# Optimization experiments

Hardware: AMD Instinct MI355X
Metric: run time of the kernel (lower is better)

Reference implementation:

```python
import jax, jax.numpy as jnp
from jax import lax
import numpy as np

B, C, T = 256, 64, 4096   # batch, in_channels, seq_len
H, K, NBLK, O = 64, 2, 4, 64  # hidden_channels, kernel, blocks, out_channels


def _conv1d(x, w, b, stride=1):
    # x: [N,C,T], w: [Cout,Cin,K], b: [Cout]
    y = lax.conv_general_dilated(x, w, window_strides=(stride,), padding='VALID',
                                 dimension_numbers=('NCH', 'OIH', 'NCH'))
    return y + b[None, :, None]


def setup_inputs() -> dict:
    key = jax.random.key(0)
    ks = jax.random.split(key, 12)
    s = 0.05  # small init so relu/sigmoid stay in sane range across 4 blocks
    return {
        'x': jax.random.normal(ks[0], (B, C, T), jnp.float32),
        'sig_w': jax.random.normal(ks[1], (NBLK, H, C, K), jnp.float32) * s,
        'sig_b': jax.random.normal(ks[2], (NBLK, H), jnp.float32) * s,
        'gate_w': jax.random.normal(ks[3], (NBLK, H, C, K), jnp.float32) * s,
        'gate_b': jax.random.normal(ks[4], (NBLK, H), jnp.float32) * s,
        'out_w': jax.random.normal(ks[5], (NBLK, C, H, 1), jnp.float32) * s,
        'out_b': jax.random.normal(ks[6], (NBLK, C), jnp.float32) * s,
        'skip_w': jax.random.normal(ks[7], (O, C, 1), jnp.float32) * s,
        'skip_b': jax.random.normal(ks[8], (O,), jnp.float32) * s,
        'dil_w': jax.random.normal(ks[9], (C, C, 2), jnp.float32) * s,
        'dil_b': jax.random.normal(ks[10], (C,), jnp.float32) * s,
    }


def reference(x, sig_w, sig_b, gate_w, gate_b, out_w, out_b,
              skip_w, skip_b, dil_w, dil_b):
    kk = sig_w.shape[-1]
    g = x
    for i in range(sig_w.shape[0]):  # fixed small number of blocks
        padded = jnp.pad(g, ((0, 0), (0, 0), (kk - 1, 0)))  # causal left-pad
        s = jax.nn.relu(_conv1d(padded, sig_w[i], sig_b[i]))
        gt = jax.nn.sigmoid(_conv1d(padded, gate_w[i], gate_b[i]))
        g = g + _conv1d(s * gt, out_w[i], out_b[i])  # 1x1 conv + residual
    dilated = _conv1d(jnp.pad(g, ((0, 0), (0, 0), (1, 0))), dil_w, dil_b, stride=2)
    skip = _conv1d(g[:, :, -1:], skip_w, skip_b)  # 1x1 conv on last step
    return dilated, skip
```

## Files before the change

### kernel.cpp

```cpp
#include <hip/hip_runtime.h>

typedef short s16x8 __attribute__((ext_vector_type(8)));
typedef short s16x4 __attribute__((ext_vector_type(4)));
typedef float f32x4 __attribute__((ext_vector_type(4)));

#define CH 64
#define TSEQ 4096
#define TOUT 2048
#define NBLK 4
#define COLS 112
#define TT 106
#define HALO 6
#define NTILE 39
#define NT 7
#define GBROW 72
#define GFROW 68
#define QPT 53
#define DIL_TOTAL 33554432

#define WA_OFF 0
#define WO_OFF 131072
#define WD_OFF 163840
#define SK_BYTE_OFF 360448

__device__ __forceinline__ short f2bf(float x) {
  unsigned u = __float_as_uint(x);
  return (short)((u + 0x7fffu + ((u >> 16) & 1u)) >> 16);
}
__device__ __forceinline__ float bf2f(short h) {
  return __uint_as_float(((unsigned)(unsigned short)h) << 16);
}
__device__ __forceinline__ f32x4 mfma16(s16x8 a, s16x8 b, f32x4 c) {
  return __builtin_amdgcn_mfma_f32_16x16x32_bf16(a, b, c, 0, 0, 0);
}

__global__ void prep(const float* __restrict__ sig_w, const float* __restrict__ gate_w,
                     const float* __restrict__ out_w, const float* __restrict__ dil_w,
                     const float* __restrict__ skip_w, short* __restrict__ wsS,
                     float* __restrict__ wsF) {
  const int idx = blockIdx.x * 256 + threadIdx.x;
  if (idx < 131072) {
    const int inner = idx & 2047, grp = idx >> 11;
    const int tap = grp & 1, kc = (grp >> 1) & 1, half = (grp >> 2) & 1;
    const int mat = (grp >> 3) & 1, blk = grp >> 4;
    const int h = inner >> 5, c = kc * 32 + (inner & 31);
    const float* W = mat ? gate_w : sig_w;
    const float w = W[((blk * CH + h) * CH + c) * 2 + tap];
    const short hi = f2bf(w);
    wsS[WA_OFF + idx] = half ? f2bf(w - bf2f(hi)) : hi;
  } else if (idx < 163840) {
    const int i2 = idx - 131072;
    const int inner = i2 & 2047, grp = i2 >> 11;
    const int kc = grp & 1, half = (grp >> 1) & 1, blk = grp >> 2;
    const int c = inner >> 5, h = kc * 32 + (inner & 31);
    const float w = out_w[(blk * CH + c) * CH + h];
    const short hi = f2bf(w);
    wsS[idx] = half ? f2bf(w - bf2f(hi)) : hi;
  } else if (idx < 180224) {
    const int i3 = idx - 163840;
    const int inner = i3 & 2047, grp = i3 >> 11;
    const int tap = grp & 1, kc = (grp >> 1) & 1, half = (grp >> 2) & 1;
    const int co = inner >> 5, ci = kc * 32 + (inner & 31);
    const float w = dil_w[(co * CH + ci) * 2 + tap];
    const short hi = f2bf(w);
    wsS[idx] = half ? f2bf(w - bf2f(hi)) : hi;
  } else if (idx < 184320) {
    const int i4 = idx - 180224;
    const int ci = i4 >> 6, o = i4 & 63;
    wsF[i4] = skip_w[o * CH + ci];
  }
}

__global__ __launch_bounds__(256, 2)
void wavenet_mfma(const float* __restrict__ x,
                  const float* __restrict__ sig_b, const float* __restrict__ gate_b,
                  const float* __restrict__ out_b, const float* __restrict__ skip_b,
                  const float* __restrict__ dil_b, const short* __restrict__ wsS,
                  const float* __restrict__ wsF, float* __restrict__ out) {
  __shared__ __align__(16) float gF[COLS * GFROW];
  __shared__ __align__(16) short GBs[2 * 113 * GBROW];

  const int tile = blockIdx.x % NTILE;
  const int b    = blockIdx.x / NTILE;
  const int t0   = tile * TT;
  const int tid  = threadIdx.x;
  const int lane = tid & 63;
  const int wv   = tid >> 6;
  const int n    = lane & 15;
  const int g4   = lane >> 4;
  const int hbase = wv * 16;

  for (int idx = tid; idx < CH * COLS; idx += 256) {
    const int c = idx / COLS, p = idx - c * COLS;
    const int tg = t0 - HALO + p;
    float v = 0.f;
    if (tg >= 0 && tg < TSEQ) v = x[(b * CH + c) * TSEQ + tg];
    gF[p * GFROW + c] = v;
    const short hi = f2bf(v);
    GBs[(p + 1) * GBROW + c] = hi;
    GBs[(113 + p + 1) * GBROW + c] = f2bf(v - bf2f(hi));
  }
  if (tid < 2 * GBROW) {
    const int half = tid / GBROW;
    GBs[half * 113 * GBROW + (tid - half * GBROW)] = 0;
  }
  __syncthreads();

  const short* bpH0 = &GBs[(n + 0) * GBROW + g4 * 8];
  const short* bpH1 = &GBs[(n + 1) * GBROW + g4 * 8];
  const short* bpL0 = &GBs[(113 + n + 0) * GBROW + g4 * 8];
  const short* bpL1 = &GBs[(113 + n + 1) * GBROW + g4 * 8];
  const int lo_p = (tile == 0) ? HALO : 0;
  const int lbase = (hbase + n) * 32 + g4 * 8;

#pragma unroll 1
  for (int blk = 0; blk < NBLK; ++blk) {
    s16x8 wS[2][2][2], wG[2][2][2], wO2[2][2];
#pragma unroll
    for (int half = 0; half < 2; ++half)
#pragma unroll
      for (int kc = 0; kc < 2; ++kc) {
#pragma unroll
        for (int tap = 0; tap < 2; ++tap) {
          wS[half][kc][tap] = *(const s16x8*)&wsS[WA_OFF + ((((blk*2+0)*2+half)*2+kc)*2+tap)*2048 + lbase];
          wG[half][kc][tap] = *(const s16x8*)&wsS[WA_OFF + ((((blk*2+1)*2+half)*2+kc)*2+tap)*2048 + lbase];
        }
        wO2[half][kc] = *(const s16x8*)&wsS[WO_OFF + ((blk*2+half)*2+kc)*2048 + lbase];
      }

    f32x4 aS[NT], aG[NT];
#pragma unroll
    for (int j = 0; j < NT; ++j) { aS[j] = (f32x4)0.f; aG[j] = (f32x4)0.f; }
#pragma unroll
    for (int j = 0; j < NT; ++j) {
      const int ro = j * 16 * GBROW;
#pragma unroll
      for (int kc = 0; kc < 2; ++kc) {
        const int co = ro + kc * 32;
        {
          const s16x8 bh = *(const s16x8*)(bpH0 + co);
          const s16x8 bl = *(const s16x8*)(bpL0 + co);
          aS[j] = mfma16(wS[0][kc][0], bh, aS[j]);
          aS[j] = mfma16(wS[1][kc][0], bh, aS[j]);
          aS[j] = mfma16(wS[0][kc][0], bl, aS[j]);
          aG[j] = mfma16(wG[0][kc][0], bh, aG[j]);
          aG[j] = mfma16(wG[1][kc][0], bh, aG[j]);
          aG[j] = mfma16(wG[0][kc][0], bl, aG[j]);
        }
        {
          const s16x8 bh = *(const s16x8*)(bpH1 + co);
          const s16x8 bl = *(const s16x8*)(bpL1 + co);
          aS[j] = mfma16(wS[0][kc][1], bh, aS[j]);
          aS[j] = mfma16(wS[1][kc][1], bh, aS[j]);
          aS[j] = mfma16(wS[0][kc][1], bl, aS[j]);
          aG[j] = mfma16(wG[0][kc][1], bh, aG[j]);
          aG[j] = mfma16(wG[1][kc][1], bh, aG[j]);
          aG[j] = mfma16(wG[0][kc][1], bl, aG[j]);
        }
      }
    }
    __syncthreads();

    const f32x4 bs4 = *(const f32x4*)(sig_b  + blk * 64 + hbase + g4 * 4);
    const f32x4 bg4 = *(const f32x4*)(gate_b + blk * 64 + hbase + g4 * 4);
#pragma unroll
    for (int j = 0; j < NT; ++j) {
      s16x4 uh, ul;
#pragma unroll
      for (int r = 0; r < 4; ++r) {
        const float s = fmaxf(aS[j][r] + bs4[r], 0.f);
        const float t = aG[j][r] + bg4[r];
        const float u = s * __builtin_amdgcn_rcpf(1.f + __expf(-t));
        const short hi = f2bf(u);
        uh[r] = hi; ul[r] = f2bf(u - bf2f(hi));
      }
      const int r1 = j * 16 + n + 1;
      *(s16x4*)&GBs[r1 * GBROW + hbase + g4 * 4] = uh;
      *(s16x4*)&GBs[(113 + r1) * GBROW + hbase + g4 * 4] = ul;
    }
    __syncthreads();

    f32x4 aO[NT];
    const f32x4 ob4 = *(const f32x4*)(out_b + blk * 64 + hbase + g4 * 4);
#pragma unroll
    for (int j = 0; j < NT; ++j) aO[j] = ob4;
#pragma unroll
    for (int j = 0; j < NT; ++j) {
      const int ro = j * 16 * GBROW;
#pragma unroll
      for (int kc = 0; kc < 2; ++kc) {
        const s16x8 uh = *(const s16x8*)(bpH1 + ro + kc * 32);
        const s16x8 ul = *(const s16x8*)(bpL1 + ro + kc * 32);
        aO[j] = mfma16(wO2[0][kc], uh, aO[j]);
        aO[j] = mfma16(wO2[1][kc], uh, aO[j]);
        aO[j] = mfma16(wO2[0][kc], ul, aO[j]);
      }
    }
    __syncthreads();

#pragma unroll
    for (int j = 0; j < NT; ++j) {
      const int p = j * 16 + n;
      float* gp = &gF[p * GFROW + hbase + g4 * 4];
      const f32x4 old = *(const f32x4*)gp;
      const f32x4 nv = (p >= lo_p) ? (old + aO[j]) : old;
      *(f32x4*)gp = nv;
      s16x4 nh, nl;
#pragma unroll
      for (int r = 0; r < 4; ++r) {
        const short hi = f2bf(nv[r]);
        nh[r] = hi; nl[r] = f2bf(nv[r] - bf2f(hi));
      }
      *(s16x4*)&GBs[(p + 1) * GBROW + hbase + g4 * 4] = nh;
      *(s16x4*)&GBs[(113 + p + 1) * GBROW + hbase + g4 * 4] = nl;
    }
    __syncthreads();
  }

  {
    s16x8 wD[2][2][2];
#pragma unroll
    for (int half = 0; half < 2; ++half)
#pragma unroll
      for (int kc = 0; kc < 2; ++kc)
#pragma unroll
        for (int tap = 0; tap < 2; ++tap)
          wD[half][kc][tap] = *(const s16x8*)&wsS[WD_OFF + ((half*2+kc)*2+tap)*2048 + lbase];
    const f32x4 db4 = *(const f32x4*)(dil_b + hbase + g4 * 4);
    const int tau0 = tile * QPT;
#pragma unroll
    for (int j = 0; j < 4; ++j) {
      const int idx = j * 16 + n;
      const int idxc = (idx < QPT) ? idx : (QPT - 1);
      f32x4 ad = db4;
      const int rbase = (6 + idxc * 2) * GBROW + g4 * 8;
#pragma unroll
      for (int kc = 0; kc < 2; ++kc)
#pragma unroll
        for (int tap = 0; tap < 2; ++tap) {
          const s16x8 bh = *(const s16x8*)&GBs[rbase + tap * GBROW + kc * 32];
          const s16x8 bl = *(const s16x8*)&GBs[113 * GBROW + rbase + tap * GBROW + kc * 32];
          ad = mfma16(wD[0][kc][tap], bh, ad);
          ad = mfma16(wD[1][kc][tap], bh, ad);
          ad = mfma16(wD[0][kc][tap], bl, ad);
        }
      const int tau = tau0 + idx;
      if (idx < QPT && tau < TOUT) {
        const int cobase = b * CH + hbase + g4 * 4;
#pragma unroll
        for (int r = 0; r < 4; ++r)
          out[(cobase + r) * TOUT + tau] = ad[r];
      }
    }
  }

  if (tile == NTILE - 1 && wv == 0) {
    const int o = lane;
    float a = skip_b[o];
    for (int c = 0; c < CH; ++c)
      a = fmaf(wsF[c * CH + o], gF[73 * GFROW + c], a);
    out[DIL_TOTAL + b * CH + o] = a;
  }
}

extern "C" void kernel_launch(void* const* d_in, const int* in_sizes, int n_in,
                              void* d_out, int out_size, void* d_ws, size_t ws_size,
                              hipStream_t stream) {
  const float* x      = (const float*)d_in[0];
  const float* sig_w  = (const float*)d_in[1];
  const float* sig_b  = (const float*)d_in[2];
  const float* gate_w = (const float*)d_in[3];
  const float* gate_b = (const float*)d_in[4];
  const float* out_w  = (const float*)d_in[5];
  const float* out_b  = (const float*)d_in[6];
  const float* skip_w = (const float*)d_in[7];
  const float* skip_b = (const float*)d_in[8];
  const float* dil_w  = (const float*)d_in[9];
  const float* dil_b  = (const float*)d_in[10];
  short* wsS = (short*)d_ws;
  float* wsF = (float*)((char*)d_ws + SK_BYTE_OFF);
  float* out = (float*)d_out;

  prep<<<dim3(720), dim3(256), 0, stream>>>(sig_w, gate_w, out_w, dil_w, skip_w, wsS, wsF);
  wavenet_mfma<<<dim3(256 * NTILE), dim3(256), 0, stream>>>(
      x, sig_b, gate_b, out_b, skip_b, dil_b, (const short*)wsS, (const float*)wsF, out);
}
```

Measured before the change: 1.202 ms.

## Keep residual stream in registers instead of LDS and raise occupancy target

Drops the fp32 shared-memory copy of the residual signal. Each thread now keeps its own 4-channel by 7-position slice in registers, which cuts the LDS footprint from about 63KB to about 33KB. Launch bounds go from 2 to 4 blocks per SM, and the out-projection weight loads move later to shorten their register lifetime. The risk is register pressure or spilling under the tighter bound. The initial x load also switches to per-thread strided reads that may coalesce less well.

```diff
diff --git a/kernel.cpp b/kernel.cpp
--- a/kernel.cpp
+++ b/kernel.cpp
@@ -14,7 +14,6 @@
 #define NTILE 39
 #define NT 7
 #define GBROW 72
-#define GFROW 68
 #define QPT 53
 #define DIL_TOTAL 33554432
 
@@ -71,14 +70,14 @@
   }
 }
 
-__global__ __launch_bounds__(256, 2)
+__global__ __launch_bounds__(256, 4)
 void wavenet_mfma(const float* __restrict__ x,
                   const float* __restrict__ sig_b, const float* __restrict__ gate_b,
                   const float* __restrict__ out_b, const float* __restrict__ skip_b,
                   const float* __restrict__ dil_b, const short* __restrict__ wsS,
                   const float* __restrict__ wsF, float* __restrict__ out) {
-  __shared__ __align__(16) float gF[COLS * GFROW];
   __shared__ __align__(16) short GBs[2 * 113 * GBROW];
+  __shared__ __align__(16) float skipBuf[CH];
 
   const int tile = blockIdx.x % NTILE;
   const int b    = blockIdx.x / NTILE;
@@ -89,16 +88,33 @@
   const int n    = lane & 15;
   const int g4   = lane >> 4;
   const int hbase = wv * 16;
-
-  for (int idx = tid; idx < CH * COLS; idx += 256) {
-    const int c = idx / COLS, p = idx - c * COLS;
-    const int tg = t0 - HALO + p;
-    float v = 0.f;
-    if (tg >= 0 && tg < TSEQ) v = x[(b * CH + c) * TSEQ + tg];
-    gF[p * GFROW + c] = v;
-    const short hi = f2bf(v);
-    GBs[(p + 1) * GBROW + c] = hi;
-    GBs[(113 + p + 1) * GBROW + c] = f2bf(v - bf2f(hi));
+  const int cch  = hbase + g4 * 4;
+
+  f32x4 gReg[NT];
+
+  {
+    const float* xb = x + ((size_t)(b * CH + cch)) * TSEQ;
+#pragma unroll
+    for (int j = 0; j < NT; ++j) {
+      const int p = j * 16 + n;
+      const int tg = t0 - HALO + p;
+      f32x4 v = (f32x4)0.f;
+      if (tg >= 0 && tg < TSEQ) {
+        v[0] = xb[tg];
+        v[1] = xb[TSEQ + tg];
+        v[2] = xb[2 * TSEQ + tg];
+        v[3] = xb[3 * TSEQ + tg];
+      }
+      gReg[j] = v;
+      s16x4 nh, nl;
+#pragma unroll
+      for (int r = 0; r < 4; ++r) {
+        const short hi = f2bf(v[r]);
+        nh[r] = hi; nl[r] = f2bf(v[r] - bf2f(hi));
+      }
+      *(s16x4*)&GBs[(p + 1) * GBROW + cch] = nh;
+      *(s16x4*)&GBs[(113 + p + 1) * GBROW + cch] = nl;
+    }
   }
   if (tid < 2 * GBROW) {
     const int half = tid / GBROW;
@@ -115,18 +131,16 @@
 
 #pragma unroll 1
   for (int blk = 0; blk < NBLK; ++blk) {
-    s16x8 wS[2][2][2], wG[2][2][2], wO2[2][2];
+    s16x8 wS[2][2][2], wG[2][2][2];
 #pragma unroll
     for (int half = 0; half < 2; ++half)
 #pragma unroll
-      for (int kc = 0; kc < 2; ++kc) {
+      for (int kc = 0; kc < 2; ++kc)
 #pragma unroll
         for (int tap = 0; tap < 2; ++tap) {
           wS[half][kc][tap] = *(const s16x8*)&wsS[WA_OFF + ((((blk*2+0)*2+half)*2+kc)*2+tap)*2048 + lbase];
           wG[half][kc][tap] = *(const s16x8*)&wsS[WA_OFF + ((((blk*2+1)*2+half)*2+kc)*2+tap)*2048 + lbase];
         }
-        wO2[half][kc] = *(const s16x8*)&wsS[WO_OFF + ((blk*2+half)*2+kc)*2048 + lbase];
-      }
 
     f32x4 aS[NT], aG[NT];
 #pragma unroll
@@ -161,8 +175,8 @@
     }
     __syncthreads();
 
-    const f32x4 bs4 = *(const f32x4*)(sig_b  + blk * 64 + hbase + g4 * 4);
-    const f32x4 bg4 = *(const f32x4*)(gate_b + blk * 64 + hbase + g4 * 4);
+    const f32x4 bs4 = *(const f32x4*)(sig_b  + blk * 64 + cch);
+    const f32x4 bg4 = *(const f32x4*)(gate_b + blk * 64 + cch);
 #pragma unroll
     for (int j = 0; j < NT; ++j) {
       s16x4 uh, ul;
@@ -175,13 +189,19 @@
         uh[r] = hi; ul[r] = f2bf(u - bf2f(hi));
       }
       const int r1 = j * 16 + n + 1;
-      *(s16x4*)&GBs[r1 * GBROW + hbase + g4 * 4] = uh;
-      *(s16x4*)&GBs[(113 + r1) * GBROW + hbase + g4 * 4] = ul;
-    }
-    __syncthreads();
-
+      *(s16x4*)&GBs[r1 * GBROW + cch] = uh;
+      *(s16x4*)&GBs[(113 + r1) * GBROW + cch] = ul;
+    }
+    __syncthreads();
+
+    s16x8 wO2[2][2];
+#pragma unroll
+    for (int half = 0; half < 2; ++half)
+#pragma unroll
+      for (int kc = 0; kc < 2; ++kc)
+        wO2[half][kc] = *(const s16x8*)&wsS[WO_OFF + ((blk*2+half)*2+kc)*2048 + lbase];
     f32x4 aO[NT];
-    const f32x4 ob4 = *(const f32x4*)(out_b + blk * 64 + hbase + g4 * 4);
+    const f32x4 ob4 = *(const f32x4*)(out_b + blk * 64 + cch);
 #pragma unroll
     for (int j = 0; j < NT; ++j) aO[j] = ob4;
 #pragma unroll
@@ -201,20 +221,22 @@
 #pragma unroll
     for (int j = 0; j < NT; ++j) {
       const int p = j * 16 + n;
-      float* gp = &gF[p * GFROW + hbase + g4 * 4];
-      const f32x4 old = *(const f32x4*)gp;
-      const f32x4 nv = (p >= lo_p) ? (old + aO[j]) : old;
-      *(f32x4*)gp = nv;
+      const f32x4 nv = (p >= lo_p) ? (f32x4)(gReg[j] + aO[j]) : gReg[j];
+      gReg[j] = nv;
       s16x4 nh, nl;
 #pragma unroll
       for (int r = 0; r < 4; ++r) {
         const short hi = f2bf(nv[r]);
         nh[r] = hi; nl[r] = f2bf(nv[r] - bf2f(hi));
       }
-      *(s16x4*)&GBs[(p + 1) * GBROW + hbase + g4 * 4] = nh;
-      *(s16x4*)&GBs[(113 + p + 1) * GBROW + hbase + g4 * 4] = nl;
-    }
-    __syncthreads();
+      *(s16x4*)&GBs[(p + 1) * GBROW + cch] = nh;
+      *(s16x4*)&GBs[(113 + p + 1) * GBROW + cch] = nl;
+    }
+    __syncthreads();
+  }
+
+  if (tile == NTILE - 1 && n == 9) {
+    *(f32x4*)&skipBuf[cch] = gReg[4];
   }
 
   {
@@ -226,7 +248,7 @@
 #pragma unroll
         for (int tap = 0; tap < 2; ++tap)
           wD[half][kc][tap] = *(const s16x8*)&wsS[WD_OFF + ((half*2+kc)*2+tap)*2048 + lbase];
-    const f32x4 db4 = *(const f32x4*)(dil_b + hbase + g4 * 4);
+    const f32x4 db4 = *(const f32x4*)(dil_b + cch);
     const int tau0 = tile * QPT;
 #pragma unroll
     for (int j = 0; j < 4; ++j) {
@@ -246,7 +268,7 @@
         }
       const int tau = tau0 + idx;
       if (idx < QPT && tau < TOUT) {
-        const int cobase = b * CH + hbase + g4 * 4;
+        const int cobase = b * CH + cch;
 #pragma unroll
         for (int r = 0; r < 4; ++r)
           out[(cobase + r) * TOUT + tau] = ad[r];
@@ -254,12 +276,15 @@
     }
   }
 
-  if (tile == NTILE - 1 && wv == 0) {
-    const int o = lane;
-    float a = skip_b[o];
-    for (int c = 0; c < CH; ++c)
-      a = fmaf(wsF[c * CH + o], gF[73 * GFROW + c], a);
-    out[DIL_TOTAL + b * CH + o] = a;
+  if (tile == NTILE - 1) {
+    __syncthreads();
+    if (wv == 0) {
+      const int o = lane;
+      float a = skip_b[o];
+      for (int c = 0; c < CH; ++c)
+        a = fmaf(wsF[c * CH + o], skipBuf[c], a);
+      out[DIL_TOTAL + b * CH + o] = a;
+    }
   }
 }
 
```

Result: slower. 1.451 ms (+20.7%).

## Replace fp32 residual LDS buffer with triple-bf16 split to fit three blocks per CU

Applied to the files above, without the earlier changes.

Removes the fp32 residual shared buffer and represents the residual stream as hi/lo/extra bf16 slices, reconstructing the old value in registers during the activation pass. This cuts LDS per block so launch bounds can request three resident blocks per CU, and defers out-projection weight loads to lower register pressure. It adds conversion ALU work and an extra LDS slice, and risks register spills under the tighter register budget.

```diff
diff --git a/kernel.cpp b/kernel.cpp
--- a/kernel.cpp
+++ b/kernel.cpp
@@ -14,7 +14,6 @@
 #define NTILE 39
 #define NT 7
 #define GBROW 72
-#define GFROW 68
 #define QPT 53
 #define DIL_TOTAL 33554432
 
@@ -71,14 +70,14 @@
   }
 }
 
-__global__ __launch_bounds__(256, 2)
+__global__ __launch_bounds__(256, 3)
 void wavenet_mfma(const float* __restrict__ x,
                   const float* __restrict__ sig_b, const float* __restrict__ gate_b,
                   const float* __restrict__ out_b, const float* __restrict__ skip_b,
                   const float* __restrict__ dil_b, const short* __restrict__ wsS,
                   const float* __restrict__ wsF, float* __restrict__ out) {
-  __shared__ __align__(16) float gF[COLS * GFROW];
   __shared__ __align__(16) short GBs[2 * 113 * GBROW];
+  __shared__ __align__(16) short GEs[113 * GBROW];
 
   const int tile = blockIdx.x % NTILE;
   const int b    = blockIdx.x / NTILE;
@@ -89,20 +88,25 @@
   const int n    = lane & 15;
   const int g4   = lane >> 4;
   const int hbase = wv * 16;
+  const int cch  = hbase + g4 * 4;
 
   for (int idx = tid; idx < CH * COLS; idx += 256) {
     const int c = idx / COLS, p = idx - c * COLS;
     const int tg = t0 - HALO + p;
     float v = 0.f;
     if (tg >= 0 && tg < TSEQ) v = x[(b * CH + c) * TSEQ + tg];
-    gF[p * GFROW + c] = v;
     const short hi = f2bf(v);
+    const float lf = v - bf2f(hi);
+    const short lo = f2bf(lf);
     GBs[(p + 1) * GBROW + c] = hi;
-    GBs[(113 + p + 1) * GBROW + c] = f2bf(v - bf2f(hi));
+    GBs[(113 + p + 1) * GBROW + c] = lo;
+    GEs[(p + 1) * GBROW + c] = f2bf(lf - bf2f(lo));
   }
   if (tid < 2 * GBROW) {
     const int half = tid / GBROW;
     GBs[half * 113 * GBROW + (tid - half * GBROW)] = 0;
+  } else if (tid < 3 * GBROW) {
+    GEs[tid - 2 * GBROW] = 0;
   }
   __syncthreads();
 
@@ -115,18 +119,16 @@
 
 #pragma unroll 1
   for (int blk = 0; blk < NBLK; ++blk) {
-    s16x8 wS[2][2][2], wG[2][2][2], wO2[2][2];
+    s16x8 wS[2][2][2], wG[2][2][2];
 #pragma unroll
     for (int half = 0; half < 2; ++half)
 #pragma unroll
-      for (int kc = 0; kc < 2; ++kc) {
+      for (int kc = 0; kc < 2; ++kc)
 #pragma unroll
         for (int tap = 0; tap < 2; ++tap) {
           wS[half][kc][tap] = *(const s16x8*)&wsS[WA_OFF + ((((blk*2+0)*2+half)*2+kc)*2+tap)*2048 + lbase];
           wG[half][kc][tap] = *(const s16x8*)&wsS[WA_OFF + ((((blk*2+1)*2+half)*2+kc)*2+tap)*2048 + lbase];
         }
-        wO2[half][kc] = *(const s16x8*)&wsS[WO_OFF + ((blk*2+half)*2+kc)*2048 + lbase];
-      }
 
     f32x4 aS[NT], aG[NT];
 #pragma unroll
@@ -161,27 +163,38 @@
     }
     __syncthreads();
 
-    const f32x4 bs4 = *(const f32x4*)(sig_b  + blk * 64 + hbase + g4 * 4);
-    const f32x4 bg4 = *(const f32x4*)(gate_b + blk * 64 + hbase + g4 * 4);
+    f32x4 gOld[NT];
+    const f32x4 bs4 = *(const f32x4*)(sig_b  + blk * 64 + cch);
+    const f32x4 bg4 = *(const f32x4*)(gate_b + blk * 64 + cch);
 #pragma unroll
     for (int j = 0; j < NT; ++j) {
+      const int r1 = j * 16 + n + 1;
+      const s16x4 oh = *(const s16x4*)&GBs[r1 * GBROW + cch];
+      const s16x4 ol = *(const s16x4*)&GBs[(113 + r1) * GBROW + cch];
+      const s16x4 oe = *(const s16x4*)&GEs[r1 * GBROW + cch];
       s16x4 uh, ul;
 #pragma unroll
       for (int r = 0; r < 4; ++r) {
+        gOld[j][r] = bf2f(oh[r]) + bf2f(ol[r]) + bf2f(oe[r]);
         const float s = fmaxf(aS[j][r] + bs4[r], 0.f);
         const float t = aG[j][r] + bg4[r];
         const float u = s * __builtin_amdgcn_rcpf(1.f + __expf(-t));
         const short hi = f2bf(u);
         uh[r] = hi; ul[r] = f2bf(u - bf2f(hi));
       }
-      const int r1 = j * 16 + n + 1;
-      *(s16x4*)&GBs[r1 * GBROW + hbase + g4 * 4] = uh;
-      *(s16x4*)&GBs[(113 + r1) * GBROW + hbase + g4 * 4] = ul;
+      *(s16x4*)&GBs[r1 * GBROW + cch] = uh;
+      *(s16x4*)&GBs[(113 + r1) * GBROW + cch] = ul;
     }
     __syncthreads();
 
+    s16x8 wO2[2][2];
+#pragma unroll
+    for (int half = 0; half < 2; ++half)
+#pragma unroll
+      for (int kc = 0; kc < 2; ++kc)
+        wO2[half][kc] = *(const s16x8*)&wsS[WO_OFF + ((blk*2+half)*2+kc)*2048 + lbase];
     f32x4 aO[NT];
-    const f32x4 ob4 = *(const f32x4*)(out_b + blk * 64 + hbase + g4 * 4);
+    const f32x4 ob4 = *(const f32x4*)(out_b + blk * 64 + cch);
 #pragma unroll
     for (int j = 0; j < NT; ++j) aO[j] = ob4;
 #pragma unroll
@@ -201,18 +214,18 @@
 #pragma unroll
     for (int j = 0; j < NT; ++j) {
       const int p = j * 16 + n;
-      float* gp = &gF[p * GFROW + hbase + g4 * 4];
-      const f32x4 old = *(const f32x4*)gp;
-      const f32x4 nv = (p >= lo_p) ? (old + aO[j]) : old;
-      *(f32x4*)gp = nv;
-      s16x4 nh, nl;
+      const f32x4 nv = (p >= lo_p) ? (f32x4)(gOld[j] + aO[j]) : gOld[j];
+      s16x4 nh, nl, ne;
 #pragma unroll
       for (int r = 0; r < 4; ++r) {
         const short hi = f2bf(nv[r]);
-        nh[r] = hi; nl[r] = f2bf(nv[r] - bf2f(hi));
-      }
-      *(s16x4*)&GBs[(p + 1) * GBROW + hbase + g4 * 4] = nh;
-      *(s16x4*)&GBs[(113 + p + 1) * GBROW + hbase + g4 * 4] = nl;
+        const float lf = nv[r] - bf2f(hi);
+        const short lo = f2bf(lf);
+        nh[r] = hi; nl[r] = lo; ne[r] = f2bf(lf - bf2f(lo));
+      }
+      *(s16x4*)&GBs[(p + 1) * GBROW + cch] = nh;
+      *(s16x4*)&GBs[(113 + p + 1) * GBROW + cch] = nl;
+      *(s16x4*)&GEs[(p + 1) * GBROW + cch] = ne;
     }
     __syncthreads();
   }
@@ -226,7 +239,7 @@
 #pragma unroll
         for (int tap = 0; tap < 2; ++tap)
           wD[half][kc][tap] = *(const s16x8*)&wsS[WD_OFF + ((half*2+kc)*2+tap)*2048 + lbase];
-    const f32x4 db4 = *(const f32x4*)(dil_b + hbase + g4 * 4);
+    const f32x4 db4 = *(const f32x4*)(dil_b + cch);
     const int tau0 = tile * QPT;
 #pragma unroll
     for (int j = 0; j < 4; ++j) {
@@ -246,7 +259,7 @@
         }
       const int tau = tau0 + idx;
       if (idx < QPT && tau < TOUT) {
-        const int cobase = b * CH + hbase + g4 * 4;
+        const int cobase = b * CH + cch;
 #pragma unroll
         for (int r = 0; r < 4; ++r)
           out[(cobase + r) * TOUT + tau] = ad[r];
@@ -257,8 +270,11 @@
   if (tile == NTILE - 1 && wv == 0) {
     const int o = lane;
     float a = skip_b[o];
-    for (int c = 0; c < CH; ++c)
-      a = fmaf(wsF[c * CH + o], gF[73 * GFROW + c], a);
+    for (int c = 0; c < CH; ++c) {
+      const float g = bf2f(GBs[74 * GBROW + c]) + bf2f(GBs[(113 + 74) * GBROW + c])
+                    + bf2f(GEs[74 * GBROW + c]);
+      a = fmaf(wsF[c * CH + o], g, a);
+    }
     out[DIL_TOTAL + b * CH + o] = a;
   }
 }
```

Result: faster. 1.116 ms (-7.2%).
